# Kernel optimization log

Measured on AMD Instinct MI355X. Metric: run time of the kernel, lower is better.

## Reference

```python
import jax, jax.numpy as jnp
import numpy as np

ALPHA = 0.2  # LeakyReLU negative slope
NEG_INF = -9e15


def setup_inputs() -> dict:
    key = jax.random.key(0)
    k1, k2, k3, k4 = jax.random.split(key, 4)
    B, N, D = 8, 2048, 256
    h = jax.random.normal(k1, (B, N, D), dtype=jnp.float32)
    adj = jax.random.randint(k2, (B, N, N), 0, 2, dtype=jnp.int32)
    W = jax.random.normal(k3, (D, D), dtype=jnp.float32) * (1.0 / np.sqrt(D))
    a = jax.random.normal(k4, (2 * D, 1), dtype=jnp.float32) * 0.05
    return {"h": h, "adj": adj, "W": W, "a": a}


def reference(h, adj, W, a):
    # Wh = Linear(h): torch nn.Linear with weight W [out,in] -> h @ W.T
    Wh = jnp.einsum('bnd,od->bno', h, W)            # [B,N,D]
    D = Wh.shape[-1]
    a1, a2 = a[:D, 0], a[D:, 0]                     # split concat-attention vector
    # e_ij = leakyrelu(a1.Wh_i + a2.Wh_j) without materializing [B,N,N,2D]
    s1 = Wh @ a1                                    # [B,N]
    s2 = Wh @ a2                                    # [B,N]
    e = jax.nn.leaky_relu(s1[:, :, None] + s2[:, None, :], negative_slope=ALPHA)
    e = jnp.where(adj > 0, e, NEG_INF)
    attention = jax.nn.softmax(e, axis=-1)          # dropout is identity in eval
    h_prime = jnp.einsum('bij,bjd->bid', attention, Wh)
    return h_prime
```

## Files before the change

### kernel.cpp

```cpp
#include <hip/hip_runtime.h>
#include <cstdint>
#include <cstddef>


#define NB 8
#define NN 2048
#define ND 256
#define ALPHA_F 0.2f
#define JC 64
#define NCH2 32
#define IR 128

typedef __attribute__((ext_vector_type(8))) short short8;
typedef __attribute__((ext_vector_type(4))) float f32x4;
typedef __attribute__((ext_vector_type(4))) int   i32x4;

__device__ __forceinline__ unsigned short f2bf(float f) {
  union { float f; unsigned int u; } v; v.f = f;
  unsigned int r = v.u + 0x7FFFu + ((v.u >> 16) & 1u);
  return (unsigned short)(r >> 16);
}

__device__ __forceinline__ short8 pack8(const float* v) {
  short8 r;
#pragma unroll
  for (int e = 0; e < 8; ++e) r[e] = (short)f2bf(v[e]);
  return r;
}

__device__ __forceinline__ unsigned int cvtpk(float lo, float hi) {
  unsigned int r;
  asm("v_cvt_pk_bf16_f32 %0, %1, %2" : "=v"(r) : "v"(lo), "v"(hi));
  return r;
}

__global__ __launch_bounds__(256) void k_wh(
    const float* __restrict__ h, const float* __restrict__ W,
    const float* __restrict__ a,
    unsigned short* __restrict__ WhT, float* __restrict__ s1g,
    float* __restrict__ s2g)
{
  __shared__ float sl1[64], sl2[64];
  const int tid  = threadIdx.x;
  const int wid  = tid >> 6;
  const int lane = tid & 63;
  const int l15  = lane & 15;
  const int c    = lane >> 4;
  const int r0   = blockIdx.x * 64;
  const int b    = r0 >> 11;
  const int n0   = r0 & 2047;

  if (tid < 64) { sl1[tid] = 0.f; sl2[tid] = 0.f; }

  f32x4 acc[4][4] = {};

  const float* hb = h + (size_t)r0 * ND;
  const int ocol0 = wid * 64;

  for (int k0 = 0; k0 < ND; k0 += 32) {
    short8 afr[4], bfr[4];
#pragma unroll
    for (int mi = 0; mi < 4; ++mi) {
      const float* p = hb + (size_t)(mi * 16 + l15) * ND + k0 + c * 8;
      float t[8];
      *(f32x4*)t       = *(const f32x4*)p;
      *(f32x4*)(t + 4) = *(const f32x4*)(p + 4);
      afr[mi] = pack8(t);
    }
#pragma unroll
    for (int ni = 0; ni < 4; ++ni) {
      const int o = ocol0 + ni * 16 + l15;
      const float* p = W + (size_t)o * ND + k0 + c * 8;
      float t[8];
      *(f32x4*)t       = *(const f32x4*)p;
      *(f32x4*)(t + 4) = *(const f32x4*)(p + 4);
      bfr[ni] = pack8(t);
    }
#pragma unroll
    for (int mi = 0; mi < 4; ++mi)
#pragma unroll
      for (int ni = 0; ni < 4; ++ni)
        acc[mi][ni] = __builtin_amdgcn_mfma_f32_16x16x32_bf16(
            afr[mi], bfr[ni], acc[mi][ni], 0, 0, 0);
  }

  float a1v[4], a2v[4];
#pragma unroll
  for (int ni = 0; ni < 4; ++ni) {
    const int o = ocol0 + ni * 16 + l15;
    a1v[ni] = a[o];
    a2v[ni] = a[ND + o];
  }
  float p1[4][4] = {}, p2[4][4] = {};
#pragma unroll
  for (int mi = 0; mi < 4; ++mi)
#pragma unroll
    for (int ni = 0; ni < 4; ++ni)
#pragma unroll
      for (int r = 0; r < 4; ++r) {
        p1[mi][r] += acc[mi][ni][r] * a1v[ni];
        p2[mi][r] += acc[mi][ni][r] * a2v[ni];
      }
#pragma unroll
  for (int m = 1; m <= 8; m <<= 1) {
#pragma unroll
    for (int mi = 0; mi < 4; ++mi)
#pragma unroll
      for (int r = 0; r < 4; ++r) {
        p1[mi][r] += __shfl_xor(p1[mi][r], m, 64);
        p2[mi][r] += __shfl_xor(p2[mi][r], m, 64);
      }
  }
  __syncthreads();
  if (l15 == 0) {
#pragma unroll
    for (int mi = 0; mi < 4; ++mi)
#pragma unroll
      for (int r = 0; r < 4; ++r) {
        atomicAdd(&sl1[mi * 16 + c * 4 + r], p1[mi][r]);
        atomicAdd(&sl2[mi * 16 + c * 4 + r], p2[mi][r]);
      }
  }

#pragma unroll
  for (int mi = 0; mi < 4; ++mi)
#pragma unroll
    for (int ni = 0; ni < 4; ++ni) {
      const int o = ocol0 + ni * 16 + l15;
      const int n = n0 + mi * 16 + c * 4;
      unsigned short u4[4];
#pragma unroll
      for (int r = 0; r < 4; ++r) u4[r] = f2bf(acc[mi][ni][r]);
      *(uint2*)(WhT + ((size_t)b * ND + o) * NN + n) = *(uint2*)u4;
    }
  __syncthreads();
  if (tid < 64) { s1g[r0 + tid] = sl1[tid]; s2g[r0 + tid] = sl2[tid]; }
}

__global__ __launch_bounds__(1024, 1) void k_attn(
    const int* __restrict__ adj, const unsigned short* __restrict__ WhT,
    const float* __restrict__ s1g, const float* __restrict__ s2g,
    float* __restrict__ out)
{
  __shared__ __align__(16) float s2s[NN];
  __shared__ __align__(16) unsigned short pbuf[2][IR * JC];
  __shared__ float lsml[IR];

  const int tid  = threadIdx.x;
  const int wid  = tid >> 6;
  const int lane = tid & 63;
  const int l15  = lane & 15;
  const int c    = lane >> 4;
  const int bid  = blockIdx.x;
  const int b    = bid & 7;
  const int i0   = (bid >> 3) * IR;

  const int row  = tid >> 3;
  const int jseg = tid & 7;
  const int gsw  = jseg ^ (row & 7);

  if (tid < IR) lsml[tid] = 0.f;
  {
    const f32x4* src = (const f32x4*)(s2g + (size_t)b * NN);
    f32x4* dst = (f32x4*)s2s;
    for (int t = tid; t < NN / 4; t += 1024) dst[t] = src[t];
  }
  const float s1r = s1g[(size_t)b * NN + i0 + row];
  const int* abt = adj + ((size_t)(b * NN + i0 + row)) * NN + jseg * 8;

  f32x4 acc[8] = {};
  float lacc = 0.f;

  const unsigned short* wb = WhT + ((size_t)b * ND + wid * 16) * NN;

  i32x4 adm[4][2];
  short8 bfr[2][2];

#define LOADADJ(CH, P)                                                       \
  { const int* ap = abt + (CH) * JC;                                         \
    adm[P][0] = *(const i32x4*)ap;                                           \
    adm[P][1] = *(const i32x4*)(ap + 4); }

#define LOADB(CH, SL)                                                        \
  {                                                                          \
    _Pragma("unroll")                                                        \
    for (int ks = 0; ks < 2; ++ks)                                           \
      bfr[SL][ks] = *(const short8*)(wb + (size_t)l15 * NN +                 \
                                     (CH) * JC + ks * 32 + c * 8);           \
  }

#define BUILDC(CH, BB, P)                                                    \
  {                                                                          \
    const float* s2p = s2s + (CH) * JC + jseg * 8;                           \
    f32x4 sa = *(const f32x4*)s2p;                                           \
    f32x4 sb = *(const f32x4*)(s2p + 4);                                     \
    float pv[8];                                                             \
    _Pragma("unroll")                                                        \
    for (int e = 0; e < 4; ++e) {                                            \
      float ev = s1r + sa[e];                                                \
      ev = fmaxf(ev, ALPHA_F * ev);                                          \
      pv[e] = (adm[P][0][e] > 0) ? __expf(ev) : 0.f;                         \
    }                                                                        \
    _Pragma("unroll")                                                        \
    for (int e = 0; e < 4; ++e) {                                            \
      float ev = s1r + sb[e];                                                \
      ev = fmaxf(ev, ALPHA_F * ev);                                          \
      pv[4 + e] = (adm[P][1][e] > 0) ? __expf(ev) : 0.f;                     \
    }                                                                        \
    lacc += ((pv[0] + pv[1]) + (pv[2] + pv[3])) +                            \
            ((pv[4] + pv[5]) + (pv[6] + pv[7]));                             \
    i32x4 pk;                                                                \
    pk[0] = (int)cvtpk(pv[0], pv[1]);                                        \
    pk[1] = (int)cvtpk(pv[2], pv[3]);                                        \
    pk[2] = (int)cvtpk(pv[4], pv[5]);                                        \
    pk[3] = (int)cvtpk(pv[6], pv[7]);                                        \
    *(i32x4*)(&pbuf[BB][0] + row * JC + gsw * 8) = pk;                       \
  }

#define CHUNK_BARRIER()                                                      \
  { asm volatile("s_waitcnt lgkmcnt(0)" ::: "memory");                       \
    __builtin_amdgcn_s_barrier(); }

  LOADADJ(0, 0)
  LOADADJ(1, 1)
  LOADADJ(2, 2)
  LOADADJ(3, 3)
  __syncthreads();

  BUILDC(0, 0, 0)
  LOADADJ(4, 0)
  LOADB(0, 0)
  CHUNK_BARRIER()

#pragma unroll
  for (int ch = 0; ch < NCH2; ++ch) {
    const int bb = ch & 1;
    const unsigned short* pbR = &pbuf[bb][0];
    if (ch + 1 < NCH2) LOADB(ch + 1, (ch + 1) & 1)
    if (ch + 1 < NCH2) {
      BUILDC(ch + 1, (ch + 1) & 1, (ch + 1) & 3)
      if (ch + 5 < NCH2) LOADADJ(ch + 5, (ch + 5) & 3)
    }
#pragma unroll
    for (int ks = 0; ks < 2; ++ks) {
#pragma unroll
      for (int mi = 0; mi < 8; ++mi) {
        short8 am = *(const short8*)(pbR + (mi * 16 + l15) * JC +
                                     (((ks * 4 + c) ^ (l15 & 7)) * 8));
        acc[mi] = __builtin_amdgcn_mfma_f32_16x16x32_bf16(
            am, bfr[bb][ks], acc[mi], 0, 0, 0);
      }
    }
    CHUNK_BARRIER()
  }

  lacc += __shfl_xor(lacc, 1, 64);
  lacc += __shfl_xor(lacc, 2, 64);
  lacc += __shfl_xor(lacc, 4, 64);
  if ((lane & 7) == 0) atomicAdd(&lsml[row], lacc);
  __syncthreads();

  float* ob = out + ((size_t)b * NN + i0) * ND + wid * 16;
#pragma unroll
  for (int mi = 0; mi < 8; ++mi)
#pragma unroll
    for (int r = 0; r < 4; ++r) {
      const int rr = mi * 16 + c * 4 + r;
      const float linv = 1.0f / lsml[rr];
      ob[(size_t)rr * ND + l15] = acc[mi][r] * linv;
    }
#undef BUILDC
#undef LOADB
#undef LOADADJ
#undef CHUNK_BARRIER
}

extern "C" void kernel_launch(void* const* d_in, const int* in_sizes, int n_in,
                              void* d_out, int out_size, void* d_ws, size_t ws_size,
                              hipStream_t stream) {
  const float* h   = (const float*)d_in[0];
  const int*   adj = (const int*)d_in[1];
  const float* W   = (const float*)d_in[2];
  const float* a   = (const float*)d_in[3];
  float* out = (float*)d_out;

  unsigned short* WhT = (unsigned short*)d_ws;
  float* s1g = (float*)((char*)d_ws + (size_t)NB * ND * NN * 2);
  float* s2g = s1g + (size_t)NB * NN;

  k_wh<<<dim3(NB * NN / 64), dim3(256), 0, stream>>>(h, W, a, WhT, s1g, s2g);
  k_attn<<<dim3(NB * NN / IR), dim3(1024), 0, stream>>>(adj, WhT, s1g, s2g, out);
}
```

Measured before the change: 71.81 us.

## Split attention j-range across two blocks with atomic accumulation and separate normalize

Doubles the attention grid by splitting the neighbour (j) dimension into two halves, so twice as many blocks run to fill the available compute units. Partial numerators and softmax denominators are accumulated into global memory with float atomics, and a new small kernel divides each output row by its summed denominator. This adds memsets of the output and sum buffers, atomic traffic and an extra launch, and makes accumulation order nondeterministic.

```diff
diff --git a/kernel.cpp b/kernel.cpp
--- a/kernel.cpp
+++ b/kernel.cpp
@@ -8,7 +8,7 @@
 #define ND 256
 #define ALPHA_F 0.2f
 #define JC 64
-#define NCH2 32
+#define NCH 16
 #define IR 128
 
 typedef __attribute__((ext_vector_type(8))) short short8;
@@ -140,11 +140,10 @@
 __global__ __launch_bounds__(1024, 1) void k_attn(
     const int* __restrict__ adj, const unsigned short* __restrict__ WhT,
     const float* __restrict__ s1g, const float* __restrict__ s2g,
-    float* __restrict__ out)
+    float* __restrict__ lsumg, float* __restrict__ out)
 {
-  __shared__ __align__(16) float s2s[NN];
+  __shared__ __align__(16) float s2s[NN / 2];
   __shared__ __align__(16) unsigned short pbuf[2][IR * JC];
-  __shared__ float lsml[IR];
 
   const int tid  = threadIdx.x;
   const int wid  = tid >> 6;
@@ -153,25 +152,27 @@
   const int c    = lane >> 4;
   const int bid  = blockIdx.x;
   const int b    = bid & 7;
-  const int i0   = (bid >> 3) * IR;
+  const int rb   = (bid >> 3) & 15;
+  const int jg   = bid >> 7;
+  const int i0   = rb * IR;
+  const int jgbase = jg * (NN / 2);
 
   const int row  = tid >> 3;
   const int jseg = tid & 7;
   const int gsw  = jseg ^ (row & 7);
 
-  if (tid < IR) lsml[tid] = 0.f;
   {
-    const f32x4* src = (const f32x4*)(s2g + (size_t)b * NN);
+    const f32x4* src = (const f32x4*)(s2g + (size_t)b * NN + jgbase);
     f32x4* dst = (f32x4*)s2s;
-    for (int t = tid; t < NN / 4; t += 1024) dst[t] = src[t];
+    if (tid < NN / 2 / 4) dst[tid] = src[tid];
   }
   const float s1r = s1g[(size_t)b * NN + i0 + row];
-  const int* abt = adj + ((size_t)(b * NN + i0 + row)) * NN + jseg * 8;
+  const int* abt = adj + ((size_t)(b * NN + i0 + row)) * NN + jgbase + jseg * 8;
 
   f32x4 acc[8] = {};
   float lacc = 0.f;
 
-  const unsigned short* wb = WhT + ((size_t)b * ND + wid * 16) * NN;
+  const unsigned short* wb = WhT + ((size_t)b * ND + wid * 16) * NN + jgbase;
 
   i32x4 adm[4][2];
   short8 bfr[2][2];
@@ -233,13 +234,13 @@
   CHUNK_BARRIER()
 
 #pragma unroll
-  for (int ch = 0; ch < NCH2; ++ch) {
+  for (int ch = 0; ch < NCH; ++ch) {
     const int bb = ch & 1;
     const unsigned short* pbR = &pbuf[bb][0];
-    if (ch + 1 < NCH2) LOADB(ch + 1, (ch + 1) & 1)
-    if (ch + 1 < NCH2) {
+    if (ch + 1 < NCH) LOADB(ch + 1, (ch + 1) & 1)
+    if (ch + 1 < NCH) {
       BUILDC(ch + 1, (ch + 1) & 1, (ch + 1) & 3)
-      if (ch + 5 < NCH2) LOADADJ(ch + 5, (ch + 5) & 3)
+      if (ch + 5 < NCH) LOADADJ(ch + 5, (ch + 5) & 3)
     }
 #pragma unroll
     for (int ks = 0; ks < 2; ++ks) {
@@ -257,8 +258,8 @@
   lacc += __shfl_xor(lacc, 1, 64);
   lacc += __shfl_xor(lacc, 2, 64);
   lacc += __shfl_xor(lacc, 4, 64);
-  if ((lane & 7) == 0) atomicAdd(&lsml[row], lacc);
-  __syncthreads();
+  if ((lane & 7) == 0)
+    atomicAdd(&lsumg[(size_t)b * NN + i0 + row], lacc);
 
   float* ob = out + ((size_t)b * NN + i0) * ND + wid * 16;
 #pragma unroll
@@ -266,13 +267,24 @@
 #pragma unroll
     for (int r = 0; r < 4; ++r) {
       const int rr = mi * 16 + c * 4 + r;
-      const float linv = 1.0f / lsml[rr];
-      ob[(size_t)rr * ND + l15] = acc[mi][r] * linv;
+      atomicAdd(&ob[(size_t)rr * ND + l15], acc[mi][r]);
     }
 #undef BUILDC
 #undef LOADB
 #undef LOADADJ
 #undef CHUNK_BARRIER
+}
+
+__global__ __launch_bounds__(256) void k_div(
+    float* __restrict__ out, const float* __restrict__ lsumg)
+{
+  const int t  = threadIdx.x;
+  const int rr = blockIdx.x * 4 + (t >> 6);
+  const float linv = 1.0f / lsumg[rr];
+  f32x4* o = (f32x4*)(out + (size_t)rr * ND) + (t & 63);
+  f32x4 v = *o;
+  v[0] *= linv; v[1] *= linv; v[2] *= linv; v[3] *= linv;
+  *o = v;
 }
 
 extern "C" void kernel_launch(void* const* d_in, const int* in_sizes, int n_in,
@@ -287,7 +299,12 @@
   unsigned short* WhT = (unsigned short*)d_ws;
   float* s1g = (float*)((char*)d_ws + (size_t)NB * ND * NN * 2);
   float* s2g = s1g + (size_t)NB * NN;
+  float* lsumg = s2g + (size_t)NB * NN;
+
+  hipMemsetAsync(d_out, 0, (size_t)out_size * sizeof(float), stream);
+  hipMemsetAsync(lsumg, 0, (size_t)NB * NN * sizeof(float), stream);
 
   k_wh<<<dim3(NB * NN / 64), dim3(256), 0, stream>>>(h, W, a, WhT, s1g, s2g);
-  k_attn<<<dim3(NB * NN / IR), dim3(1024), 0, stream>>>(adj, WhT, s1g, s2g, out);
-}
+  k_attn<<<dim3(256), dim3(1024), 0, stream>>>(adj, WhT, s1g, s2g, lsumg, out);
+  k_div<<<dim3(NB * NN / 4), dim3(256), 0, stream>>>(out, lsumg);
+}
```

Result: slower. 91.20 us (+27.0%).
